# Kernel tuning notes

Hardware: AMD Instinct MI355X
Metric: run time of the kernel (lower is better)

## Reference

```python
import jax, jax.numpy as jnp
import numpy as np

NUM_CAV = 62000            # CAVs in the ragged batch
K = 3                      # past frames per object


def _counts():
    # deterministic ragged counts in [1, 31]; sum = 2000 * 496 = 992000 objects
    return ((np.arange(NUM_CAV) % 31) + 1).astype(np.int32)


def setup_inputs() -> dict:
    key = jax.random.key(0)
    k1, k2 = jax.random.split(key)
    counts = _counts()
    n_obj = int(counts.sum())  # 992000
    # [N, 3, 7] past 7-dof boxes; only [..., :2] (x, y) is used
    past_k_object_bbx = jax.random.normal(k1, (n_obj, K, 7), dtype=jnp.float32) * 10.0
    # strictly increasing timestamps per CAV so frame-to-frame dt != 0
    dt = jax.random.uniform(k2, (NUM_CAV, K), dtype=jnp.float32, minval=0.05, maxval=0.2)
    past_k_time_interval = jnp.cumsum(dt, axis=1).reshape(-1)  # flat, view(-1,3) compatible
    past_k_object_cav_num = jnp.asarray(counts)
    return {
        'past_k_object_bbx': past_k_object_bbx,
        'past_k_time_interval': past_k_time_interval,
        'past_k_object_cav_num': past_k_object_cav_num,
    }


def reference(past_k_object_bbx, past_k_time_interval, past_k_object_cav_num):
    # Faithful vectorization of extract_date_backup1 (j-indexed replicate loop ==
    # repeat_interleave of per-CAV time rows to per-object rows).
    n_obj = past_k_object_bbx.shape[0]
    # time grid per CAV, reversed so index -1 is the most recent frame
    td = jnp.flip(past_k_time_interval.reshape(-1, K), axis=1)        # [C, 3]
    coords = jnp.flip(past_k_object_bbx[:, :, :2], axis=1)           # [N, 3, 2]
    coords = coords - coords[:, -1:, :]                               # normalize to last frame
    # ragged row replication -> gather via cumulative offsets
    offsets = jnp.cumsum(past_k_object_cav_num)                       # [C]
    cav_idx = jnp.searchsorted(offsets, jnp.arange(n_obj), side='right')
    td_rep = td[cav_idx]                                              # [N, 3]
    td_norm = td_rep - td_rep[:, -1:]                                  # [N, 3]
    dt = td_rep[:, 1:] - td_rep[:, :-1]                                # [N, 2] (time_encode)
    distance = coords[:, 1:, :] - coords[:, :-1, :]                    # [N, 2, 2]
    speed = distance / dt[..., None]                                   # [N, 2, 2]
    obj_input = jnp.concatenate([distance, speed], axis=-1)[None]      # [1, N, 2, 4]
    # linear extrapolation of last motion to t = 0 (the 'query')
    last_len = td_norm[:, -1] - td_norm[:, -2]                          # [N]
    safe_len = jnp.where(last_len == 0, jnp.float32(1.0), last_len)
    extrap = coords[:, -1, :] + (coords[:, -1, :] - coords[:, -2, :]) * (-td_rep[:, -1:]) / safe_len[:, None]
    query = jnp.where((last_len == 0)[:, None], jnp.float32(0.0), extrap).reshape(1, n_obj, 1, 2)
    target_time_diff = -td_rep[:, -1]                                  # [N]
    time_encode = dt                                                   # [N, 2]
    return obj_input, query, time_encode, target_time_diff
```

## Files before the change

### kernel.cpp

```cpp
#include <hip/hip_runtime.h>
#include <stdint.h>

#define SCAN_BS 1024
#define OBJ_BS  256
#define SLAB_F  (OBJ_BS * 21)
#define SLAB_CH (SLAB_F / 256)
#define WIN     257
#define SOFF_CH 5

__device__ __forceinline__ void gload_lds16(const void* g, void* l) {
    __builtin_amdgcn_global_load_lds(
        (const __attribute__((address_space(1))) uint32_t*)g,
        (__attribute__((address_space(3))) uint32_t*)l, 16, 0, 0);
}
__device__ __forceinline__ void gload_lds4(const void* g, void* l) {
    __builtin_amdgcn_global_load_lds(
        (const __attribute__((address_space(1))) uint32_t*)g,
        (__attribute__((address_space(3))) uint32_t*)l, 4, 0, 0);
}


__global__ __launch_bounds__(SCAN_BS) void scan_fused_kernel(
    const int* __restrict__ counts, int C,
    int* __restrict__ offsets, int* __restrict__ blockCav) {

    __shared__ int sdata[SCAN_BS];
    __shared__ int wsum[SCAN_BS / 64];

    const int tid  = threadIdx.x;
    const int lane = tid & 63;
    const int wid  = tid >> 6;
    const int b    = blockIdx.x;
    const int gid  = b * SCAN_BS + tid;
    const int chunkStart = b * SCAN_BS;

    const int v = (gid < C) ? counts[gid] : 0;
    sdata[tid] = v;

    int csum = 0;
    for (int idx = tid; idx < chunkStart; idx += SCAN_BS) csum += counts[idx];
    #pragma unroll
    for (int o = 32; o > 0; o >>= 1) csum += __shfl_down(csum, o, 64);
    if (lane == 0) wsum[wid] = csum;
    __syncthreads();

    for (int ofs = 1; ofs < SCAN_BS; ofs <<= 1) {
        int add = (tid >= ofs) ? sdata[tid - ofs] : 0;
        __syncthreads();
        sdata[tid] += add;
        __syncthreads();
    }

    int carry = 0;
    #pragma unroll
    for (int w = 0; w < SCAN_BS / 64; ++w) carry += wsum[w];

    if (gid < C) {
        const int end = sdata[tid] + carry;
        offsets[gid] = end;
        const int start = end - v;
        int s0 = ((start + OBJ_BS - 1) / OBJ_BS) * OBJ_BS;
        for (int s = s0; s < end; s += OBJ_BS) blockCav[s / OBJ_BS] = gid;
    }
}


__global__ __launch_bounds__(OBJ_BS) void motion_kernel(
    const float* __restrict__ bbx, const float* __restrict__ tint,
    const int* __restrict__ offsets, const int* __restrict__ blockCav,
    int C, int N, float* __restrict__ out) {

    __shared__ __align__(16) float sb[SLAB_F];
    __shared__ int soff[SOFF_CH * 64];

    const int tid  = threadIdx.x;
    const int lane = tid & 63;
    const int wid  = tid >> 6;
    const long long blockStart = (long long)blockIdx.x * OBJ_BS;
    const int nObjBlk = (int)min((long long)OBJ_BS, (long long)N - blockStart);

    const int c_lo = blockCav[blockIdx.x];

    const float* gsrc = bbx + blockStart * 21;
    if (nObjBlk == OBJ_BS) {
        #pragma unroll
        for (int ch = wid; ch < SLAB_CH; ch += 4)
            gload_lds16((const void*)(gsrc + ch * 256 + lane * 4), (void*)(sb + ch * 256));
    } else {
        const int nElem = nObjBlk * 21;
        for (int k = tid; k < nElem; k += OBJ_BS) sb[k] = gsrc[k];
    }

    int c0 = min(c_lo, C - WIN); if (c0 < 0) c0 = 0;
    if (wid == 0) {
        #pragma unroll
        for (int ch = 0; ch < SOFF_CH; ++ch)
            gload_lds4((const void*)(offsets + c0 + ch * 64 + lane), (void*)(soff + ch * 64));
    }

    __syncthreads();

    if (tid >= nObjBlk) return;
    const int i = (int)(blockStart + tid);

    int lo = 0, hi = WIN;
    while (lo < hi) {
        int mid = (lo + hi) >> 1;
        if (soff[mid] > i) hi = mid; else lo = mid + 1;
    }
    const int cav = c0 + lo;

    const float t0 = tint[3 * cav + 0];
    const float t1 = tint[3 * cav + 1];
    const float t2 = tint[3 * cav + 2];

    const float dt0 = t1 - t2;
    const float dt1 = t0 - t1;

    const float* bp = sb + tid * 21;
    const float x0 = bp[0],  y0 = bp[1];
    const float x1 = bp[7],  y1 = bp[8];
    const float x2 = bp[14], y2 = bp[15];

    const float c0x = x2 - x0, c0y = y2 - y0;
    const float c1x = x1 - x0, c1y = y1 - y0;

    const float d0x = c1x - c0x, d0y = c1y - c0y;
    const float d1x = 0.0f - c1x, d1y = 0.0f - c1y;

    const float s0x = d0x / dt0, s0y = d0y / dt0;
    const float s1x = d1x / dt1, s1y = d1y / dt1;

    const float last_len = 0.0f - (t1 - t0);
    const float safe_len = (last_len == 0.0f) ? 1.0f : last_len;
    const float exx = ((0.0f - c1x) * (0.0f - t0)) / safe_len;
    const float exy = ((0.0f - c1y) * (0.0f - t0)) / safe_len;
    const float qx = (last_len == 0.0f) ? 0.0f : exx;
    const float qy = (last_len == 0.0f) ? 0.0f : exy;

    const size_t Ns = (size_t)N;
    float4* oi = (float4*)out;
    oi[(size_t)i * 2 + 0] = make_float4(d0x, d0y, s0x, s0y);
    oi[(size_t)i * 2 + 1] = make_float4(d1x, d1y, s1x, s1y);

    float2* q  = (float2*)(out + 8 * Ns);
    q[i] = make_float2(qx, qy);

    float2* te = (float2*)(out + 10 * Ns);
    te[i] = make_float2(dt0, dt1);

    out[12 * Ns + (size_t)i] = 0.0f - t0;
}


extern "C" void kernel_launch(void* const* d_in, const int* in_sizes, int n_in,
                              void* d_out, int out_size, void* d_ws, size_t ws_size,
                              hipStream_t stream) {
    const float* bbx  = (const float*)d_in[0];
    const float* tint = (const float*)d_in[1];
    const int*   cnt  = (const int*)d_in[2];
    float* out = (float*)d_out;

    const int N = in_sizes[0] / 21;
    const int C = in_sizes[2];

    const int nb  = (C + SCAN_BS - 1) / SCAN_BS;
    const int nob = (N + OBJ_BS - 1) / OBJ_BS;

    int* offsets  = (int*)d_ws;
    int* blockCav = offsets + C + 64;

    scan_fused_kernel<<<nb, SCAN_BS, 0, stream>>>(cnt, C, offsets, blockCav);
    motion_kernel<<<nob, OBJ_BS, 0, stream>>>(bbx, tint, offsets, blockCav, C, N, out);
}
```

Baseline: 38.89 us.

## Scatter per-object CAV index in scan kernel instead of binary search

The scan kernel now writes the CAV index for every object into a dense per-object array, replacing the offsets array and per-block starting CAV. The motion kernel loads that index directly instead of staging a window of offsets in LDS and binary searching it, and issues the time loads before the barrier so they overlap the slab load. This removes the per-thread search but adds a serial per-CAV write loop of up to 31 scattered stores in the scan kernel, plus roughly 4 MB of extra index traffic.

```diff
diff --git a/kernel.cpp b/kernel.cpp
--- a/kernel.cpp
+++ b/kernel.cpp
@@ -5,24 +5,17 @@
 #define OBJ_BS  256
 #define SLAB_F  (OBJ_BS * 21)
 #define SLAB_CH (SLAB_F / 256)
-#define WIN     257
-#define SOFF_CH 5
 
 __device__ __forceinline__ void gload_lds16(const void* g, void* l) {
     __builtin_amdgcn_global_load_lds(
         (const __attribute__((address_space(1))) uint32_t*)g,
         (__attribute__((address_space(3))) uint32_t*)l, 16, 0, 0);
 }
-__device__ __forceinline__ void gload_lds4(const void* g, void* l) {
-    __builtin_amdgcn_global_load_lds(
-        (const __attribute__((address_space(1))) uint32_t*)g,
-        (__attribute__((address_space(3))) uint32_t*)l, 4, 0, 0);
-}
 
 
-__global__ __launch_bounds__(SCAN_BS) void scan_fused_kernel(
+__global__ __launch_bounds__(SCAN_BS) void scan_scatter_kernel(
     const int* __restrict__ counts, int C,
-    int* __restrict__ offsets, int* __restrict__ blockCav) {
+    int* __restrict__ cavIdx) {
 
     __shared__ int sdata[SCAN_BS];
     __shared__ int wsum[SCAN_BS / 64];
@@ -56,30 +49,25 @@
     for (int w = 0; w < SCAN_BS / 64; ++w) carry += wsum[w];
 
     if (gid < C) {
-        const int end = sdata[tid] + carry;
-        offsets[gid] = end;
+        const int end   = sdata[tid] + carry;
         const int start = end - v;
-        int s0 = ((start + OBJ_BS - 1) / OBJ_BS) * OBJ_BS;
-        for (int s = s0; s < end; s += OBJ_BS) blockCav[s / OBJ_BS] = gid;
+        for (int s = start; s < end; ++s) cavIdx[s] = gid;
     }
 }
 
 
 __global__ __launch_bounds__(OBJ_BS) void motion_kernel(
     const float* __restrict__ bbx, const float* __restrict__ tint,
-    const int* __restrict__ offsets, const int* __restrict__ blockCav,
-    int C, int N, float* __restrict__ out) {
+    const int* __restrict__ cavIdx, int N,
+    float* __restrict__ out) {
 
     __shared__ __align__(16) float sb[SLAB_F];
-    __shared__ int soff[SOFF_CH * 64];
 
     const int tid  = threadIdx.x;
     const int lane = tid & 63;
     const int wid  = tid >> 6;
     const long long blockStart = (long long)blockIdx.x * OBJ_BS;
     const int nObjBlk = (int)min((long long)OBJ_BS, (long long)N - blockStart);
-
-    const int c_lo = blockCav[blockIdx.x];
 
     const float* gsrc = bbx + blockStart * 21;
     if (nObjBlk == OBJ_BS) {
@@ -91,28 +79,17 @@
         for (int k = tid; k < nElem; k += OBJ_BS) sb[k] = gsrc[k];
     }
 
-    int c0 = min(c_lo, C - WIN); if (c0 < 0) c0 = 0;
-    if (wid == 0) {
-        #pragma unroll
-        for (int ch = 0; ch < SOFF_CH; ++ch)
-            gload_lds4((const void*)(offsets + c0 + ch * 64 + lane), (void*)(soff + ch * 64));
-    }
+    const int i = (int)(blockStart + tid);
+    const bool act = (tid < nObjBlk);
+
+    const int   cav = act ? cavIdx[i] : 0;
+    const float t0  = tint[3 * cav + 0];
+    const float t1  = tint[3 * cav + 1];
+    const float t2  = tint[3 * cav + 2];
 
     __syncthreads();
 
-    if (tid >= nObjBlk) return;
-    const int i = (int)(blockStart + tid);
-
-    int lo = 0, hi = WIN;
-    while (lo < hi) {
-        int mid = (lo + hi) >> 1;
-        if (soff[mid] > i) hi = mid; else lo = mid + 1;
-    }
-    const int cav = c0 + lo;
-
-    const float t0 = tint[3 * cav + 0];
-    const float t1 = tint[3 * cav + 1];
-    const float t2 = tint[3 * cav + 2];
+    if (!act) return;
 
     const float dt0 = t1 - t2;
     const float dt1 = t0 - t1;
@@ -167,9 +144,8 @@
     const int nb  = (C + SCAN_BS - 1) / SCAN_BS;
     const int nob = (N + OBJ_BS - 1) / OBJ_BS;
 
-    int* offsets  = (int*)d_ws;
-    int* blockCav = offsets + C + 64;
+    int* cavIdx = (int*)d_ws;
 
-    scan_fused_kernel<<<nb, SCAN_BS, 0, stream>>>(cnt, C, offsets, blockCav);
-    motion_kernel<<<nob, OBJ_BS, 0, stream>>>(bbx, tint, offsets, blockCav, C, N, out);
+    scan_scatter_kernel<<<nb, SCAN_BS, 0, stream>>>(cnt, C, cavIdx);
+    motion_kernel<<<nob, OBJ_BS, 0, stream>>>(bbx, tint, cavIdx, N, out);
 }
```

Measured after the change: 41.76 us. 7.4% more time.

## Use wave-shuffle scan and stage per-CAV times and offsets in LDS

Applied to the files above, without the earlier changes.

The scan kernel drops to 256-thread blocks and replaces the LDS Hillis-Steele scan, which had many barriers, with a per-wave __shfl_up scan plus a per-wave carry combine. The motion kernel now loads a window of 257 offsets starting at the block's first CAV, along with that window's time-interval triples, into LDS with coalesced loads. Each object then binary-searches this window and reads its times from LDS instead of gathering them from global memory. In exchange, the scan kernel launches four times as many blocks, and each block's serial prefix loop over earlier counts runs longer.

```diff
diff --git a/kernel.cpp b/kernel.cpp
--- a/kernel.cpp
+++ b/kernel.cpp
@@ -1,22 +1,16 @@
 #include <hip/hip_runtime.h>
+#include <limits.h>
 #include <stdint.h>
 
-#define SCAN_BS 1024
+#define SCAN_BS 256
 #define OBJ_BS  256
 #define SLAB_F  (OBJ_BS * 21)
 #define SLAB_CH (SLAB_F / 256)
-#define WIN     257
-#define SOFF_CH 5
 
 __device__ __forceinline__ void gload_lds16(const void* g, void* l) {
     __builtin_amdgcn_global_load_lds(
         (const __attribute__((address_space(1))) uint32_t*)g,
         (__attribute__((address_space(3))) uint32_t*)l, 16, 0, 0);
-}
-__device__ __forceinline__ void gload_lds4(const void* g, void* l) {
-    __builtin_amdgcn_global_load_lds(
-        (const __attribute__((address_space(1))) uint32_t*)g,
-        (__attribute__((address_space(3))) uint32_t*)l, 4, 0, 0);
 }
 
 
@@ -24,39 +18,42 @@
     const int* __restrict__ counts, int C,
     int* __restrict__ offsets, int* __restrict__ blockCav) {
 
-    __shared__ int sdata[SCAN_BS];
-    __shared__ int wsum[SCAN_BS / 64];
+    __shared__ int cw[SCAN_BS / 64];
+    __shared__ int wv[SCAN_BS / 64];
 
     const int tid  = threadIdx.x;
     const int lane = tid & 63;
     const int wid  = tid >> 6;
-    const int b    = blockIdx.x;
-    const int gid  = b * SCAN_BS + tid;
-    const int chunkStart = b * SCAN_BS;
+    const int gid  = blockIdx.x * SCAN_BS + tid;
+    const int chunkStart = blockIdx.x * SCAN_BS;
 
     const int v = (gid < C) ? counts[gid] : 0;
-    sdata[tid] = v;
 
     int csum = 0;
     for (int idx = tid; idx < chunkStart; idx += SCAN_BS) csum += counts[idx];
     #pragma unroll
     for (int o = 32; o > 0; o >>= 1) csum += __shfl_down(csum, o, 64);
-    if (lane == 0) wsum[wid] = csum;
+
+    int inc = v;
+    #pragma unroll
+    for (int o = 1; o < 64; o <<= 1) {
+        int t = __shfl_up(inc, o, 64);
+        if (lane >= o) inc += t;
+    }
+
+    if (lane == 0)  cw[wid] = csum;
+    if (lane == 63) wv[wid] = inc;
     __syncthreads();
 
-    for (int ofs = 1; ofs < SCAN_BS; ofs <<= 1) {
-        int add = (tid >= ofs) ? sdata[tid - ofs] : 0;
-        __syncthreads();
-        sdata[tid] += add;
-        __syncthreads();
+    int base = 0;
+    #pragma unroll
+    for (int w = 0; w < SCAN_BS / 64; ++w) {
+        base += cw[w];
+        if (w < wid) base += wv[w];
     }
 
-    int carry = 0;
-    #pragma unroll
-    for (int w = 0; w < SCAN_BS / 64; ++w) carry += wsum[w];
-
     if (gid < C) {
-        const int end = sdata[tid] + carry;
+        const int end = base + inc;
         offsets[gid] = end;
         const int start = end - v;
         int s0 = ((start + OBJ_BS - 1) / OBJ_BS) * OBJ_BS;
@@ -71,7 +68,8 @@
     int C, int N, float* __restrict__ out) {
 
     __shared__ __align__(16) float sb[SLAB_F];
-    __shared__ int soff[SOFF_CH * 64];
+    __shared__ int   soff[OBJ_BS + 1];
+    __shared__ float st[3 * (OBJ_BS + 1)];
 
     const int tid  = threadIdx.x;
     const int lane = tid & 63;
@@ -91,36 +89,50 @@
         for (int k = tid; k < nElem; k += OBJ_BS) sb[k] = gsrc[k];
     }
 
-    int c0 = min(c_lo, C - WIN); if (c0 < 0) c0 = 0;
-    if (wid == 0) {
-        #pragma unroll
-        for (int ch = 0; ch < SOFF_CH; ++ch)
-            gload_lds4((const void*)(offsets + c0 + ch * 64 + lane), (void*)(soff + ch * 64));
+    const int c = c_lo + tid;
+    const int offv = (c < C) ? offsets[c] : INT_MAX;
+    int off_last = INT_MAX;
+    if (tid == 0) {
+        int c2 = c_lo + OBJ_BS;
+        off_last = (c2 < C) ? offsets[c2] : INT_MAX;
     }
+    const int base3 = 3 * c_lo;
+    const int lim3  = 3 * C - base3;
+    const float tv0 = (tid < lim3)       ? tint[base3 + tid]       : 0.0f;
+    const float tv1 = (tid + 256 < lim3) ? tint[base3 + tid + 256] : 0.0f;
+    const float tv2 = (tid + 512 < lim3) ? tint[base3 + tid + 512] : 0.0f;
+    float tv3 = 0.0f;
+    if (tid < 3 && tid + 768 < lim3) tv3 = tint[base3 + tid + 768];
+
+    soff[tid] = offv;
+    if (tid == 0) soff[OBJ_BS] = off_last;
+    st[tid]       = tv0;
+    st[tid + 256] = tv1;
+    st[tid + 512] = tv2;
+    if (tid < 3) st[tid + 768] = tv3;
 
     __syncthreads();
 
     if (tid >= nObjBlk) return;
     const int i = (int)(blockStart + tid);
 
-    int lo = 0, hi = WIN;
+    int lo = 0, hi = OBJ_BS + 1;
     while (lo < hi) {
         int mid = (lo + hi) >> 1;
         if (soff[mid] > i) hi = mid; else lo = mid + 1;
     }
-    const int cav = c0 + lo;
-
-    const float t0 = tint[3 * cav + 0];
-    const float t1 = tint[3 * cav + 1];
-    const float t2 = tint[3 * cav + 2];
+    const int j = lo;
+    const float t0 = st[3 * j + 0];
+    const float t1 = st[3 * j + 1];
+    const float t2 = st[3 * j + 2];
 
     const float dt0 = t1 - t2;
     const float dt1 = t0 - t1;
 
-    const float* bp = sb + tid * 21;
-    const float x0 = bp[0],  y0 = bp[1];
-    const float x1 = bp[7],  y1 = bp[8];
-    const float x2 = bp[14], y2 = bp[15];
+    const float* b = sb + tid * 21;
+    const float x0 = b[0],  y0 = b[1];
+    const float x1 = b[7],  y1 = b[8];
+    const float x2 = b[14], y2 = b[15];
 
     const float c0x = x2 - x0, c0y = y2 - y0;
     const float c1x = x1 - x0, c1y = y1 - y0;
```

After: 59.78 us. 1.54x slower.
